# Kernel optimization log

Hardware: AMD Instinct MI355X
Metric: run time of the kernel (lower is better)

The kernel has to match this reference:

```python
import jax, jax.numpy as jnp
import numpy as np

N = 8192
D = 256  # hidden_size = in_features = out_features
NEG_SLOPE = 0.01  # nn.LeakyReLU() default
MASK_VAL = -1e12


def setup_inputs() -> dict:
    key = jax.random.key(0)
    k1, k2, k3, k4 = jax.random.split(key, 4)
    x = jax.random.normal(k1, (N, D), dtype=jnp.float32)
    adj = jax.random.randint(k2, (N, N), 0, 2, dtype=jnp.int32)
    # kaiming_uniform_ style params (scaled random uniform)
    W = jax.random.normal(k3, (D, D), dtype=jnp.float32) * (1.0 / np.sqrt(D))
    a = jax.random.normal(k4, (2 * D, 1), dtype=jnp.float32) * (1.0 / np.sqrt(2 * D))
    return {"x": x, "adj": adj, "W": W, "a": a}


def reference(x, adj, W, a):
    # GraphAttentionLayer.forward (eval mode: dropout is identity)
    h = x @ W  # [N, D]
    # a_input[i,j] = concat(h_i, h_j); a_input @ a decomposes as:
    #   e[i,j] = h_i . a[:D] + h_j . a[D:]
    # identical math without materializing the [N, N, 2D] tensor.
    e_src = h @ a[:D, 0]  # [N]
    e_dst = h @ a[D:, 0]  # [N]
    e = e_src[:, None] + e_dst[None, :]  # [N, N]
    e = jnp.where(e > 0, e, NEG_SLOPE * e)  # LeakyReLU
    att_logits = jnp.where(adj > 0, e, MASK_VAL)
    attention = jax.nn.softmax(att_logits, axis=1)
    h_prime = attention @ h  # [N, D]
    return jax.nn.elu(h_prime)  # concat=True branch
```

## Files before the change

### kernel.cpp

```cpp
#include <hip/hip_runtime.h>

#define NN 8192
#define DD 256
#define BM 256
#define JSPLIT 8
#define JC (NN / JSPLIT)
#define NT (JC / 32)

typedef __attribute__((ext_vector_type(8))) short short8;
typedef __attribute__((ext_vector_type(4))) float f32x4;

__device__ __forceinline__ short f2bf(float x) {
    union { float f; unsigned u; } v; v.f = x;
    unsigned r = (v.u + 0x7FFFu + ((v.u >> 16) & 1u)) >> 16;
    return (short)r;
}
__device__ __forceinline__ float bf2f(short b) {
    union { float f; unsigned u; } v; v.u = ((unsigned)(unsigned short)b) << 16;
    return v.f;
}

__device__ __forceinline__ void barrier_keep_vmem() {
    asm volatile("s_waitcnt lgkmcnt(0)" ::: "memory");
    __builtin_amdgcn_s_barrier();
    asm volatile("" ::: "memory");
}

__global__ __launch_bounds__(256) void gat_pack(
    const int* __restrict__ adj, unsigned* __restrict__ bits)
{
    const int t   = threadIdx.x;
    const int row = blockIdx.x;
    const int* ar = adj + (size_t)row * NN;
    unsigned* br  = bits + (size_t)row * (NN / 32);
    #pragma unroll
    for (int i = 0; i < 8; ++i) {
        int j0 = i * 1024 + t * 4;
        int4 v = *(const int4*)(ar + j0);
        unsigned nib = (v.x > 0 ? 1u : 0u) | (v.y > 0 ? 2u : 0u)
                     | (v.z > 0 ? 4u : 0u) | (v.w > 0 ? 8u : 0u);
        unsigned word = nib << ((t & 7) * 4);
        word |= __shfl_xor((int)word, 1);
        word |= __shfl_xor((int)word, 2);
        word |= __shfl_xor((int)word, 4);
        if ((t & 7) == 0) br[i * 32 + (t >> 3)] = word;
    }
}

__global__ __launch_bounds__(256) void gat_prep(
    const float* __restrict__ x, const float* __restrict__ W,
    const float* __restrict__ a,
    short* __restrict__ hT, float* __restrict__ e_src, float* __restrict__ e_dst)
{
    __shared__ float x_s[32][260];
    __shared__ float W_s[2][16][256];
    const int t  = threadIdx.x;
    const int ib = blockIdx.x * 32;

    #pragma unroll
    for (int rep = 0; rep < 8; ++rep) {
        int fi = rep * 256 + t;
        int r  = fi >> 6;
        int c4 = (fi & 63) * 4;
        float4 v = *(const float4*)(x + (size_t)(ib + r) * DD + c4);
        *(float4*)&x_s[r][c4] = v;
    }
    float4 wp[4];
    #pragma unroll
    for (int q = 0; q < 4; ++q) {
        int fi = q * 256 + t;
        wp[q] = *(const float4*)(W + (size_t)(fi >> 6) * DD + (fi & 63) * 4);
    }
    barrier_keep_vmem();

    const int il = t >> 3;
    const int dg = (t & 7) * 4;
    f32x4 acc[8];
    #pragma unroll
    for (int m = 0; m < 8; ++m) acc[m] = (f32x4){0.f, 0.f, 0.f, 0.f};

    for (int kc = 0; kc < 16; ++kc) {
        const int b = kc & 1;
        #pragma unroll
        for (int q = 0; q < 4; ++q) {
            int fi = q * 256 + t;
            *(float4*)&W_s[b][fi >> 6][(fi & 63) * 4] = wp[q];
        }
        if (kc < 15) {
            #pragma unroll
            for (int q = 0; q < 4; ++q) {
                int fi = q * 256 + t;
                wp[q] = *(const float4*)(W + (size_t)((kc + 1) * 16 + (fi >> 6)) * DD + (fi & 63) * 4);
            }
        }
        barrier_keep_vmem();
        #pragma unroll
        for (int kl = 0; kl < 16; ++kl) {
            float xv = x_s[il][kc * 16 + kl];
            #pragma unroll
            for (int m = 0; m < 8; ++m) {
                float4 wv = *(const float4*)&W_s[b][kl][m * 32 + dg];
                acc[m].x += xv * wv.x; acc[m].y += xv * wv.y;
                acc[m].z += xv * wv.z; acc[m].w += xv * wv.w;
            }
        }
    }

    const int ig = ib + il;
    float p1 = 0.f, p2 = 0.f;
    #pragma unroll
    for (int m = 0; m < 8; ++m) {
        #pragma unroll
        for (int j = 0; j < 4; ++j) {
            int col = m * 32 + dg + j;
            float hv = acc[m][j];
            p1 += hv * a[col];
            p2 += hv * a[DD + col];
            hT[(size_t)col * NN + ig] = f2bf(hv);
        }
    }
    p1 += __shfl_xor(p1, 1); p1 += __shfl_xor(p1, 2); p1 += __shfl_xor(p1, 4);
    p2 += __shfl_xor(p2, 1); p2 += __shfl_xor(p2, 2); p2 += __shfl_xor(p2, 4);
    if ((t & 7) == 0) { e_src[ig] = p1; e_dst[ig] = p2; }
}

__global__ __launch_bounds__(512, 2) void gat_main(
    const unsigned* __restrict__ bits, const short* __restrict__ hT,
    const float* __restrict__ e_src, const float* __restrict__ e_dst,
    float* __restrict__ num, float* __restrict__ den_part)
{
    const int t    = threadIdx.x;
    const int lane = t & 63;
    const int w    = t >> 6;
    const int jc   = blockIdx.x & (JSPLIT - 1);
    const int rb   = blockIdx.x >> 3;
    const int jbase = jc * JC;
    const int rowq = w & 3;
    const int colh = w >> 2;
    const int arow = lane & 15;
    const int kg8  = (lane >> 4) * 8;
    const int rbase = rb * BM + rowq * 64;

    float es[4];
    const unsigned* brp[4];
    #pragma unroll
    for (int rt = 0; rt < 4; ++rt) {
        es[rt]  = e_src[rbase + rt * 16 + arow];
        brp[rt] = bits + (size_t)(rbase + rt * 16 + arow) * (NN / 32) + (jbase >> 5);
    }
    const float* edp = e_dst + jbase + kg8;
    const short* hB  = hT + (size_t)(colh * 128 + arow) * NN + jbase + kg8;

    f32x4 acc[4][8];
    #pragma unroll
    for (int rt = 0; rt < 4; ++rt)
        #pragma unroll
        for (int q = 0; q < 8; ++q) acc[rt][q] = (f32x4){0.f, 0.f, 0.f, 0.f};
    float ds[4] = {0.f, 0.f, 0.f, 0.f};

    unsigned bw[4];
    #pragma unroll
    for (int rt = 0; rt < 4; ++rt) bw[rt] = brp[rt][0];
    float4 e0 = *(const float4*)(edp);
    float4 e1 = *(const float4*)(edp + 4);

    for (int n = 0; n < NT; ++n) {
        const int j32 = n * 32;
        int4 bq[8];
        #pragma unroll
        for (int q = 0; q < 8; ++q)
            bq[q] = *(const int4*)(hB + (size_t)q * 16 * NN + j32);

        float ed[8] = {e0.x, e0.y, e0.z, e0.w, e1.x, e1.y, e1.z, e1.w};
        short8 af[4];
        #pragma unroll
        for (int rt = 0; rt < 4; ++rt) {
            #pragma unroll
            for (int i = 0; i < 8; ++i) {
                float s = es[rt] + ed[i];
                float l = s > 0.f ? s : 0.01f * s;
                float wv = ((bw[rt] >> (kg8 + i)) & 1u) ? __expf(l) : 0.f;
                short b = f2bf(wv);
                af[rt][i] = b;
                ds[rt] += bf2f(b);
            }
        }
        if (n + 1 < NT) {
            #pragma unroll
            for (int rt = 0; rt < 4; ++rt) bw[rt] = brp[rt][n + 1];
            e0 = *(const float4*)(edp + j32 + 32);
            e1 = *(const float4*)(edp + j32 + 36);
        }
        #pragma unroll
        for (int rt = 0; rt < 4; ++rt)
            #pragma unroll
            for (int q = 0; q < 8; ++q)
                acc[rt][q] = __builtin_amdgcn_mfma_f32_16x16x32_bf16(
                    af[rt], *(short8*)&bq[q], acc[rt][q], 0, 0, 0);
    }

    #pragma unroll
    for (int rt = 0; rt < 4; ++rt) {
        float d = ds[rt];
        d += __shfl_xor(d, 16);
        d += __shfl_xor(d, 32);
        if (colh == 0 && lane < 16)
            den_part[(size_t)jc * NN + rbase + rt * 16 + lane] = d;
    }

    float* np = num + (size_t)jc * NN * DD;
    const int r4 = (lane >> 4) * 4;
    #pragma unroll
    for (int rt = 0; rt < 4; ++rt)
        #pragma unroll
        for (int q = 0; q < 8; ++q) {
            size_t o = (size_t)(rbase + rt * 16 + r4) * DD + colh * 128 + q * 16 + arow;
            #pragma unroll
            for (int r = 0; r < 4; ++r)
                np[o + (size_t)r * DD] = acc[rt][q][r];
        }
}

__global__ __launch_bounds__(256) void gat_epi(
    float* __restrict__ out, const float* __restrict__ num,
    const float* __restrict__ den_part)
{
    int idx = blockIdx.x * 256 + threadIdx.x;
    int row = idx >> 6;
    float d = 0.f;
    #pragma unroll
    for (int p = 0; p < JSPLIT; ++p) d += den_part[(size_t)p * NN + row];
    float4 s = {0.f, 0.f, 0.f, 0.f};
    #pragma unroll
    for (int p = 0; p < JSPLIT; ++p) {
        float4 v = ((const float4*)(num + (size_t)p * NN * DD))[idx];
        s.x += v.x; s.y += v.y; s.z += v.z; s.w += v.w;
    }
    float inv = 1.f / d;
    float4 o;
    o.x = s.x * inv; o.x = o.x > 0.f ? o.x : expm1f(o.x);
    o.y = s.y * inv; o.y = o.y > 0.f ? o.y : expm1f(o.y);
    o.z = s.z * inv; o.z = o.z > 0.f ? o.z : expm1f(o.z);
    o.w = s.w * inv; o.w = o.w > 0.f ? o.w : expm1f(o.w);
    ((float4*)out)[idx] = o;
}

extern "C" void kernel_launch(void* const* d_in, const int* in_sizes, int n_in,
                              void* d_out, int out_size, void* d_ws, size_t ws_size,
                              hipStream_t stream) {
    const float* x   = (const float*)d_in[0];
    const int*   adj = (const int*)d_in[1];
    const float* W   = (const float*)d_in[2];
    const float* a   = (const float*)d_in[3];
    float* out = (float*)d_out;

    char* w0 = (char*)d_ws;
    short* hT      = (short*)w0;
    float* esrc    = (float*)(w0 + (size_t)DD * NN * 2);
    float* edst    = esrc + NN;
    unsigned* bits = (unsigned*)(edst + NN);
    float* den     = (float*)((char*)bits + (size_t)NN * (NN / 32) * 4);
    float* num     = den + (size_t)JSPLIT * NN;

    gat_pack<<<dim3(NN), dim3(256), 0, stream>>>(adj, bits);
    gat_prep<<<dim3(NN / 32), dim3(256), 0, stream>>>(x, W, a, hT, esrc, edst);
    gat_main<<<dim3((NN / BM) * JSPLIT), dim3(512), 0, stream>>>(
        bits, hT, esrc, edst, num, den);
    gat_epi<<<dim3(NN * DD / 4 / 256), dim3(256), 0, stream>>>(out, num, den);
}
```

Baseline: 211.4 us.

## Fuse adjacency packing into main kernel with LDS double-buffered hT staging

Removes the separate bit-packing kernel so the main kernel reads the int32 adjacency matrix directly, with register prefetch one step ahead. The hT tile is staged into LDS with asynchronous global_load_lds into a swizzled double buffer, so all waves share it instead of each loading its own copy. Block shape changes to 128 rows by 4 column splits, and the k-loop is pipelined with barriers. This saves one pass over adj and the bits round trip, but the main kernel now streams 256MB of int32 adj, and adds synchronisation and register pressure.

```diff
diff --git a/kernel.cpp b/kernel.cpp
--- a/kernel.cpp
+++ b/kernel.cpp
@@ -2,10 +2,11 @@
 
 #define NN 8192
 #define DD 256
-#define BM 256
-#define JSPLIT 8
-#define JC (NN / JSPLIT)
-#define NT (JC / 32)
+#define BM 128
+#define BK 64
+#define JSPLIT 4
+#define JCH (NN / JSPLIT)
+#define NT (JCH / BK)
 
 typedef __attribute__((ext_vector_type(8))) short short8;
 typedef __attribute__((ext_vector_type(4))) float f32x4;
@@ -24,27 +25,6 @@
     asm volatile("s_waitcnt lgkmcnt(0)" ::: "memory");
     __builtin_amdgcn_s_barrier();
     asm volatile("" ::: "memory");
-}
-
-__global__ __launch_bounds__(256) void gat_pack(
-    const int* __restrict__ adj, unsigned* __restrict__ bits)
-{
-    const int t   = threadIdx.x;
-    const int row = blockIdx.x;
-    const int* ar = adj + (size_t)row * NN;
-    unsigned* br  = bits + (size_t)row * (NN / 32);
-    #pragma unroll
-    for (int i = 0; i < 8; ++i) {
-        int j0 = i * 1024 + t * 4;
-        int4 v = *(const int4*)(ar + j0);
-        unsigned nib = (v.x > 0 ? 1u : 0u) | (v.y > 0 ? 2u : 0u)
-                     | (v.z > 0 ? 4u : 0u) | (v.w > 0 ? 8u : 0u);
-        unsigned word = nib << ((t & 7) * 4);
-        word |= __shfl_xor((int)word, 1);
-        word |= __shfl_xor((int)word, 2);
-        word |= __shfl_xor((int)word, 4);
-        if ((t & 7) == 0) br[i * 32 + (t >> 3)] = word;
-    }
 }
 
 __global__ __launch_bounds__(256) void gat_prep(
@@ -125,99 +105,157 @@
 }
 
 __global__ __launch_bounds__(512, 2) void gat_main(
-    const unsigned* __restrict__ bits, const short* __restrict__ hT,
+    const int* __restrict__ adj, const short* __restrict__ hT,
     const float* __restrict__ e_src, const float* __restrict__ e_dst,
     float* __restrict__ num, float* __restrict__ den_part)
 {
+    __shared__ __align__(16) short Bt[2][256 * BK];
+
     const int t    = threadIdx.x;
     const int lane = t & 63;
     const int w    = t >> 6;
+    const int wr   = w >> 2;
+    const int wc   = w & 3;
     const int jc   = blockIdx.x & (JSPLIT - 1);
-    const int rb   = blockIdx.x >> 3;
-    const int jbase = jc * JC;
-    const int rowq = w & 3;
-    const int colh = w >> 2;
+    const int rb   = blockIdx.x >> 2;
+    const int jb   = jc * JCH;
+
     const int arow = lane & 15;
-    const int kg8  = (lane >> 4) * 8;
-    const int rbase = rb * BM + rowq * 64;
+    const int kq   = lane >> 4;
+    const int kg8  = kq * 8;
+    const int cb   = wc * 64;
+    const int rbl  = rb * BM + wr * 64;
+
+    const int lrow = lane >> 3;
+    const int lblk = lane & 7;
 
     float es[4];
-    const unsigned* brp[4];
-    #pragma unroll
-    for (int rt = 0; rt < 4; ++rt) {
-        es[rt]  = e_src[rbase + rt * 16 + arow];
-        brp[rt] = bits + (size_t)(rbase + rt * 16 + arow) * (NN / 32) + (jbase >> 5);
-    }
-    const float* edp = e_dst + jbase + kg8;
-    const short* hB  = hT + (size_t)(colh * 128 + arow) * NN + jbase + kg8;
-
-    f32x4 acc[4][8];
-    #pragma unroll
-    for (int rt = 0; rt < 4; ++rt)
-        #pragma unroll
-        for (int q = 0; q < 8; ++q) acc[rt][q] = (f32x4){0.f, 0.f, 0.f, 0.f};
+    const int* arp[4];
+    #pragma unroll
+    for (int mrt = 0; mrt < 4; ++mrt) {
+        int r = rbl + mrt * 16 + arow;
+        es[mrt]  = e_src[r];
+        arp[mrt] = adj + (size_t)r * NN + jb + kg8;
+    }
+    const float* pep = e_dst + jb + kg8;
+
+    f32x4 acc[4][4];
+    #pragma unroll
+    for (int mrt = 0; mrt < 4; ++mrt)
+        #pragma unroll
+        for (int nb = 0; nb < 4; ++nb) acc[mrt][nb] = (f32x4){0.f, 0.f, 0.f, 0.f};
     float ds[4] = {0.f, 0.f, 0.f, 0.f};
 
-    unsigned bw[4];
-    #pragma unroll
-    for (int rt = 0; rt < 4; ++rt) bw[rt] = brp[rt][0];
-    float4 e0 = *(const float4*)(edp);
-    float4 e1 = *(const float4*)(edp + 4);
-
-    for (int n = 0; n < NT; ++n) {
-        const int j32 = n * 32;
-        int4 bq[8];
-        #pragma unroll
-        for (int q = 0; q < 8; ++q)
-            bq[q] = *(const int4*)(hB + (size_t)q * 16 * NN + j32);
-
-        float ed[8] = {e0.x, e0.y, e0.z, e0.w, e1.x, e1.y, e1.z, e1.w};
-        short8 af[4];
-        #pragma unroll
-        for (int rt = 0; rt < 4; ++rt) {
-            #pragma unroll
-            for (int i = 0; i < 8; ++i) {
-                float s = es[rt] + ed[i];
-                float l = s > 0.f ? s : 0.01f * s;
-                float wv = ((bw[rt] >> (kg8 + i)) & 1u) ? __expf(l) : 0.f;
-                short b = f2bf(wv);
-                af[rt][i] = b;
-                ds[rt] += bf2f(b);
-            }
-        }
-        if (n + 1 < NT) {
-            #pragma unroll
-            for (int rt = 0; rt < 4; ++rt) bw[rt] = brp[rt][n + 1];
-            e0 = *(const float4*)(edp + j32 + 32);
-            e1 = *(const float4*)(edp + j32 + 36);
-        }
-        #pragma unroll
-        for (int rt = 0; rt < 4; ++rt)
-            #pragma unroll
-            for (int q = 0; q < 8; ++q)
-                acc[rt][q] = __builtin_amdgcn_mfma_f32_16x16x32_bf16(
-                    af[rt], *(short8*)&bq[q], acc[rt][q], 0, 0, 0);
-    }
-
-    #pragma unroll
-    for (int rt = 0; rt < 4; ++rt) {
-        float d = ds[rt];
-        d += __shfl_xor(d, 16);
-        d += __shfl_xor(d, 32);
-        if (colh == 0 && lane < 16)
-            den_part[(size_t)jc * NN + rbase + rt * 16 + lane] = d;
+    int4   pa[4][2][2];
+    float4 pe[2][2];
+    short8 af[4][2];
+
+#define STAGE(b_, n_) do {                                                      \
+        int jt_ = jb + (n_) * BK;                                               \
+        _Pragma("unroll")                                                       \
+        for (int q = 0; q < 4; ++q) {                                           \
+            int d_ = w * 32 + q * 8 + lrow;                                     \
+            const short* src_ = hT + (size_t)d_ * NN + jt_ + ((lblk ^ (d_ & 7)) * 8); \
+            __builtin_amdgcn_global_load_lds(                                   \
+                (const __attribute__((address_space(1))) void*)src_,            \
+                (__attribute__((address_space(3))) void*)&Bt[b_][(w * 32 + q * 8) * BK], \
+                16, 0, 0);                                                      \
+        }                                                                       \
+        __builtin_amdgcn_sched_barrier(0);                                      \
+    } while (0)
+
+#define PREFETCH(n_) do {                                                       \
+        int j0_ = (n_) * BK;                                                    \
+        _Pragma("unroll")                                                       \
+        for (int mrt = 0; mrt < 4; ++mrt)                                       \
+            _Pragma("unroll")                                                   \
+            for (int kt = 0; kt < 2; ++kt) {                                    \
+                pa[mrt][kt][0] = *(const int4*)(arp[mrt] + j0_ + kt * 32);      \
+                pa[mrt][kt][1] = *(const int4*)(arp[mrt] + j0_ + kt * 32 + 4);  \
+            }                                                                   \
+        _Pragma("unroll")                                                       \
+        for (int kt = 0; kt < 2; ++kt) {                                        \
+            pe[kt][0] = *(const float4*)(pep + j0_ + kt * 32);                  \
+            pe[kt][1] = *(const float4*)(pep + j0_ + kt * 32 + 4);              \
+        }                                                                       \
+    } while (0)
+
+#define ABUILD do {                                                             \
+        _Pragma("unroll")                                                       \
+        for (int mrt = 0; mrt < 4; ++mrt)                                       \
+            _Pragma("unroll")                                                   \
+            for (int kt = 0; kt < 2; ++kt) {                                    \
+                const int*   av = (const int*)&pa[mrt][kt][0];                  \
+                const float* ev = (const float*)&pe[kt][0];                     \
+                _Pragma("unroll")                                               \
+                for (int i = 0; i < 8; ++i) {                                   \
+                    float s = es[mrt] + ev[i];                                  \
+                    float l = s > 0.f ? s : 0.01f * s;                          \
+                    float wv = av[i] > 0 ? __expf(l) : 0.f;                     \
+                    short bb = f2bf(wv);                                        \
+                    af[mrt][kt][i] = bb;                                        \
+                    ds[mrt] += bf2f(bb);         \
+                }                                                               \
+            }                                                                   \
+    } while (0)
+
+#define COMPUTE(b_) do {                                                        \
+        _Pragma("unroll")                                                       \
+        for (int nb = 0; nb < 4; ++nb) {                                        \
+            int d_ = cb + nb * 16 + arow;                                       \
+            const short* rowp_ = &Bt[b_][d_ * BK];                              \
+            _Pragma("unroll")                                                   \
+            for (int kt = 0; kt < 2; ++kt) {                                    \
+                short8 bf = *(const short8*)(rowp_ + (((kt * 4 + kq) ^ (arow & 7)) * 8)); \
+                _Pragma("unroll")                                               \
+                for (int mrt = 0; mrt < 4; ++mrt)                               \
+                    acc[mrt][nb] = __builtin_amdgcn_mfma_f32_16x16x32_bf16(     \
+                        af[mrt][kt], bf, acc[mrt][nb], 0, 0, 0);                \
+            }                                                                   \
+        }                                                                       \
+    } while (0)
+
+#define KSTEP(CUR, n_) do {                                                     \
+        STAGE(CUR ^ 1, ((n_) + 1) & (NT - 1));                                  \
+        ABUILD;                                                                 \
+        PREFETCH(((n_) + 1) & (NT - 1));                                        \
+        asm volatile("s_waitcnt vmcnt(24)" ::: "memory");                       \
+        __builtin_amdgcn_s_barrier();                                           \
+        asm volatile("" ::: "memory");                                          \
+        COMPUTE(CUR);                                                           \
+        barrier_keep_vmem();                                                    \
+    } while (0)
+
+    STAGE(0, 0);
+    PREFETCH(0);
+    for (int n = 0; n < NT; n += 2) {
+        KSTEP(0, n);
+        KSTEP(1, n + 1);
+    }
+#undef KSTEP
+#undef COMPUTE
+#undef ABUILD
+#undef PREFETCH
+#undef STAGE
+
+    #pragma unroll
+    for (int mrt = 0; mrt < 4; ++mrt) {
+        float dd = ds[mrt];
+        dd += __shfl_xor(dd, 16);
+        dd += __shfl_xor(dd, 32);
+        if (wc == 0 && lane < 16)
+            den_part[(size_t)jc * NN + rbl + mrt * 16 + lane] = dd;
     }
 
     float* np = num + (size_t)jc * NN * DD;
-    const int r4 = (lane >> 4) * 4;
-    #pragma unroll
-    for (int rt = 0; rt < 4; ++rt)
-        #pragma unroll
-        for (int q = 0; q < 8; ++q) {
-            size_t o = (size_t)(rbase + rt * 16 + r4) * DD + colh * 128 + q * 16 + arow;
+    #pragma unroll
+    for (int mrt = 0; mrt < 4; ++mrt)
+        #pragma unroll
+        for (int nb = 0; nb < 4; ++nb) {
+            size_t o = (size_t)(rbl + mrt * 16 + kq * 4) * DD + cb + nb * 16 + arow;
             #pragma unroll
             for (int r = 0; r < 4; ++r)
-                np[o + (size_t)r * DD] = acc[rt][q][r];
+                np[o + (size_t)r * DD] = acc[mrt][nb][r];
         }
 }
 
@@ -255,16 +293,14 @@
     float* out = (float*)d_out;
 
     char* w0 = (char*)d_ws;
-    short* hT      = (short*)w0;
-    float* esrc    = (float*)(w0 + (size_t)DD * NN * 2);
-    float* edst    = esrc + NN;
-    unsigned* bits = (unsigned*)(edst + NN);
-    float* den     = (float*)((char*)bits + (size_t)NN * (NN / 32) * 4);
-    float* num     = den + (size_t)JSPLIT * NN;
-
-    gat_pack<<<dim3(NN), dim3(256), 0, stream>>>(adj, bits);
+    short* hT   = (short*)w0;
+    float* esrc = (float*)(w0 + (size_t)DD * NN * 2);
+    float* edst = esrc + NN;
+    float* den  = edst + NN;
+    float* num  = den + (size_t)JSPLIT * NN;
+
     gat_prep<<<dim3(NN / 32), dim3(256), 0, stream>>>(x, W, a, hT, esrc, edst);
     gat_main<<<dim3((NN / BM) * JSPLIT), dim3(512), 0, stream>>>(
-        bits, hT, esrc, edst, num, den);
+        adj, hT, esrc, edst, num, den);
     gat_epi<<<dim3(NN * DD / 4 / 256), dim3(256), 0, stream>>>(out, num, den);
 }
```

Result: slower. 369.9 us (+75.0%).
